# Performance work log

Hardware: AMD Instinct MI355X
Metric: run time of the kernel (lower is better)

Reference implementation:

```python
import jax, jax.numpy as jnp
import numpy as np

DIM = 768
NUM_HEADS = 12
DECAY_RATE = 5.0


def setup_inputs() -> dict:
    key = jax.random.key(0)
    k1, k2, k3, k4 = jax.random.split(key, 4)
    B, N, C = 4, 1024, DIM
    x = jax.random.normal(k1, (B, N, C), dtype=jnp.float32)
    # torch nn.Linear weights: y = x @ W.T ; qkv_bias=False
    qkv_w = jax.random.normal(k2, (3 * C, C), dtype=jnp.float32) * (1.0 / np.sqrt(C))
    proj_w = jax.random.normal(k3, (C, C), dtype=jnp.float32) * (1.0 / np.sqrt(C))
    proj_b = jax.random.normal(k4, (C,), dtype=jnp.float32) * 0.01
    return {"x": x, "qkv_w": qkv_w, "proj_w": proj_w, "proj_b": proj_b, "cur_epoch": 3}


def reference(x, qkv_w, proj_w, proj_b, cur_epoch):
    B, N, C = x.shape
    H = NUM_HEADS
    hd = C // H
    scale = hd ** -0.5

    qkv = (x @ qkv_w.T).reshape(B, N, 3, H, hd).transpose(2, 0, 3, 1, 4)  # [3,B,H,N,hd]
    q, k, v = qkv[0], qkv[1], qkv[2]

    scores = jnp.einsum("bhqd,bhkd->bhqk", q, k) * scale
    logp = jax.nn.log_softmax(scores, axis=-1)
    attn = jnp.exp(logp)  # [B,H,N,N]

    # Per-key entropy: column j of attn flattened over (B,H,N) is renormalized
    # by Categorical; dividing by num_heads cancels under normalization.
    # H(p/s) = log(s) - (1/s) * sum(p * log p)
    s = jnp.sum(attn, axis=(0, 1, 2))                 # [N]
    plogp = jnp.sum(attn * logp, axis=(0, 1, 2))      # [N]
    entropies = jnp.log(s) - plogp / s

    # threshold decay: factor = sum_{i=0}^{cur_epoch-1} decay*exp(-(i+1))
    factor = DECAY_RATE * float(np.sum(np.exp(-(np.arange(cur_epoch) + 1.0))))
    entropy_threshold = float(np.log(C)) - factor

    # attn[:,:,:,keep] @ v[:,:,keep,:] == (attn * mask) @ v  (zeroed columns drop out)
    mask = (entropies <= entropy_threshold).astype(attn.dtype)  # [N]
    out = jnp.einsum("bhqk,bhkd->bhqd", attn * mask[None, None, None, :], v)
    out = out.transpose(0, 2, 1, 3).reshape(B, N, C)
    out = out @ proj_w.T + proj_b
    return out
```

## Files before the change

### kernel.cpp

```cpp
#include <hip/hip_runtime.h>


typedef __bf16 bf16x8 __attribute__((ext_vector_type(8)));
typedef __bf16 bf16x4 __attribute__((ext_vector_type(4)));
typedef float  f32x4  __attribute__((ext_vector_type(4)));

#define MFMA16(a, b, c) __builtin_amdgcn_mfma_f32_16x16x32_bf16((a), (b), (c), 0, 0, 0)
#define LOG2E_8 0.18033688f

__device__ __forceinline__ void ld_glds16(const __bf16* g, __bf16* s) {
  __builtin_amdgcn_global_load_lds(
      (const __attribute__((address_space(1))) unsigned int*)g,
      (__attribute__((address_space(3))) unsigned int*)s, 16, 0, 0);
}

__global__ __launch_bounds__(256) void kc_conv(
    const float* __restrict__ x, const float* __restrict__ qw, const float* __restrict__ pw,
    __bf16* __restrict__ xb, __bf16* __restrict__ qwb, __bf16* __restrict__ pwb,
    float* __restrict__ colSP, int* __restrict__ keepCnt)
{
  const int i = blockIdx.x * 256 + threadIdx.x;
  const float4* src;
  __bf16* dst;
  int j;
  if (i < 786432)       { src = (const float4*)x;  dst = xb;  j = i; }
  else if (i < 1228800) { src = (const float4*)qw; dst = qwb; j = i - 786432; }
  else                  { src = (const float4*)pw; dst = pwb; j = i - 1228800; }
  const float4 f = src[j];
  bf16x4 o;
  o[0] = (__bf16)f.x; o[1] = (__bf16)f.y; o[2] = (__bf16)f.z; o[3] = (__bf16)f.w;
  *(bf16x4*)(dst + 4 * (size_t)j) = o;
  if (i < 2048) colSP[i] = 0.f;
  if (i == 0) *keepCnt = 0;
}

__global__ __launch_bounds__(256) void kg_qkv(
    const __bf16* __restrict__ A, const __bf16* __restrict__ Bm,
    __bf16* __restrict__ qb, __bf16* __restrict__ kb, float* __restrict__ v)
{
  __shared__ __bf16 As[128 * 64];
  __shared__ __bf16 Bs[128 * 64];
  const int tid = threadIdx.x;
  const int w = tid >> 6, lane = tid & 63, quad = lane >> 4, l = lane & 15;
  const int wm = w >> 1, wn = w & 1;
  const int r0 = blockIdx.y * 128, c0 = blockIdx.x * 128;
  const int srow = lane >> 3, skk = (lane & 7) * 8;

  f32x4 acc[4][4] = {};

  for (int k0 = 0; k0 < 768; k0 += 64) {
    if (k0) __syncthreads();
#pragma unroll
    for (int s = 0; s < 4; ++s) {
      const int si = w * 4 + s;
      const int row = si * 8 + srow;
      ld_glds16(A + (size_t)(r0 + row) * 768 + k0 + skk, &As[si * 512]);
      ld_glds16(Bm + (size_t)(c0 + row) * 768 + k0 + skk, &Bs[si * 512]);
    }
    __syncthreads();
#pragma unroll
    for (int kk = 0; kk < 2; ++kk) {
      bf16x8 af[4], bf[4];
#pragma unroll
      for (int t = 0; t < 4; ++t) {
        af[t] = *(const bf16x8*)&As[(wm * 64 + t * 16 + l) * 64 + kk * 32 + quad * 8];
        bf[t] = *(const bf16x8*)&Bs[(wn * 64 + t * 16 + l) * 64 + kk * 32 + quad * 8];
      }
#pragma unroll
      for (int mt = 0; mt < 4; ++mt)
#pragma unroll
        for (int nt = 0; nt < 4; ++nt)
          acc[mt][nt] = MFMA16(af[mt], bf[nt], acc[mt][nt]);
    }
  }

  const int part = c0 / 768;
  const int cbase = c0 % 768;
#pragma unroll
  for (int mt = 0; mt < 4; ++mt) {
#pragma unroll
    for (int nt = 0; nt < 4; ++nt) {
      const int cc = cbase + wn * 64 + nt * 16 + l;
      const int h = cc >> 6, d = cc & 63;
#pragma unroll
      for (int i = 0; i < 4; ++i) {
        const int rg = r0 + wm * 64 + mt * 16 + quad * 4 + i;
        const int b_ = rg >> 10, n = rg & 1023;
        const size_t off = ((size_t)(b_ * 12 + h) * 1024 + n) * 64 + d;
        const float val = acc[mt][nt][i];
        if (part == 0)      qb[off] = (__bf16)val;
        else if (part == 1) kb[off] = (__bf16)val;
        else                v[off]  = val;
      }
    }
  }
}

__global__ __launch_bounds__(512) void ks_fused(
    const __bf16* __restrict__ qb, const __bf16* __restrict__ kb,
    float* __restrict__ lse, float* __restrict__ colSP)
{
  __shared__ float sS[1024];
  __shared__ float sP[1024];
  __shared__ float zrow[64];
  const int tid = threadIdx.x;
  const int w = tid >> 6, lane = tid & 63, quad = lane >> 4, l = lane & 15;
  const int bh = blockIdx.x, r0 = blockIdx.y * 64;
  for (int i = tid; i < 1024; i += 512) { sS[i] = 0.f; sP[i] = 0.f; }
  if (tid < 64) zrow[tid] = 0.f;
  __syncthreads();

  const __bf16* qbase = qb + ((size_t)bh * 1024 + r0 + l) * 64;
  bf16x8 aq0[4], aq1[4];
#pragma unroll
  for (int rt = 0; rt < 4; ++rt) {
    aq0[rt] = *(const bf16x8*)(qbase + rt * 1024 + quad * 8);
    aq1[rt] = *(const bf16x8*)(qbase + rt * 1024 + 32 + quad * 8);
  }
  const __bf16* kfrag = kb + (size_t)bh * 65536 + (size_t)(w * 16 + l) * 64 + quad * 8;
  const f32x4 zero = {0.f, 0.f, 0.f, 0.f};

  bf16x8 kf0 = *(const bf16x8*)(kfrag);
  bf16x8 kf1 = *(const bf16x8*)(kfrag + 32);

  float z[16] = {};
  for (int s = 0; s < 8; ++s) {
    const bf16x8 c0 = kf0, c1 = kf1;
    const int nxt = (s + 1) & 7;
    kf0 = *(const bf16x8*)(kfrag + (size_t)nxt * 8192);
    kf1 = *(const bf16x8*)(kfrag + (size_t)nxt * 8192 + 32);
#pragma unroll
    for (int rt = 0; rt < 4; ++rt) {
      f32x4 acc = MFMA16(aq0[rt], c0, zero);
      acc = MFMA16(aq1[rt], c1, acc);
#pragma unroll
      for (int r = 0; r < 4; ++r) z[rt * 4 + r] += exp2f(acc[r] * LOG2E_8);
    }
  }
#pragma unroll
  for (int off = 1; off < 16; off <<= 1) {
#pragma unroll
    for (int i = 0; i < 16; ++i) z[i] += __shfl_xor(z[i], off);
  }
  if (l == 0) {
#pragma unroll
    for (int rt = 0; rt < 4; ++rt)
#pragma unroll
      for (int r = 0; r < 4; ++r)
        atomicAdd(&zrow[rt * 16 + quad * 4 + r], z[rt * 4 + r]);
  }
  __syncthreads();
  if (tid < 64) lse[bh * 1024 + r0 + tid] = __logf(zrow[tid]);
  float nlb[16], nlg[16];
#pragma unroll
  for (int rt = 0; rt < 4; ++rt) {
#pragma unroll
    for (int r = 0; r < 4; ++r) {
      const float Z = zrow[rt * 16 + quad * 4 + r];
      const float lg = __logf(Z);
      nlg[rt * 4 + r] = -lg;
      nlb[rt * 4 + r] = -lg * 1.44269504f;
    }
  }

  for (int s = 0; s < 8; ++s) {
    const bf16x8 c0 = kf0, c1 = kf1;
    if (s < 7) {
      kf0 = *(const bf16x8*)(kfrag + (size_t)(s + 1) * 8192);
      kf1 = *(const bf16x8*)(kfrag + (size_t)(s + 1) * 8192 + 32);
    }
    float cs = 0.f, cp = 0.f;
#pragma unroll
    for (int rt = 0; rt < 4; ++rt) {
      f32x4 acc = MFMA16(aq0[rt], c0, zero);
      acc = MFMA16(aq1[rt], c1, acc);
#pragma unroll
      for (int r = 0; r < 4; ++r) {
        const float a = acc[r];
        const float t = exp2f(fmaf(a, LOG2E_8, nlb[rt * 4 + r]));
        const float d = fmaf(a, 0.125f, nlg[rt * 4 + r]);
        cs += t;
        cp = fmaf(t, d, cp);
      }
    }
    cs += __shfl_xor(cs, 16); cs += __shfl_xor(cs, 32);
    cp += __shfl_xor(cp, 16); cp += __shfl_xor(cp, 32);
    if (lane < 16) {
      sS[s * 128 + w * 16 + l] += cs;
      sP[s * 128 + w * 16 + l] += cp;
    }
  }
  __syncthreads();
  for (int i = tid; i < 1024; i += 512) {
    atomicAdd(&colSP[i], sS[i]);
    atomicAdd(&colSP[1024 + i], sP[i]);
  }
}

__global__ void k_mask(const float* __restrict__ colSP, const int* __restrict__ cur_epoch,
                       float* __restrict__ mask, int* __restrict__ keepCnt)
{
  const int j = threadIdx.x;
  const float s = colSP[j];
  const float ent = __logf(s) - colSP[1024 + j] / s;
  const int ce = cur_epoch[0];
  float factor = 0.f;
  for (int i = 1; i <= ce; ++i) factor += __expf(-(float)i);
  factor *= 5.0f;
  const float thr = __logf(768.0f) - factor;
  const int keep = (ent <= thr) ? 1 : 0;
  mask[j] = keep ? 1.0f : 0.0f;
  if (keep) atomicAdd(keepCnt, 1);
}

__global__ __launch_bounds__(256) void k_av(
    const __bf16* __restrict__ qb, const __bf16* __restrict__ kb,
    const float* __restrict__ v, const float* __restrict__ lse,
    const float* __restrict__ mask, const int* __restrict__ keepCnt,
    __bf16* __restrict__ ctxb)
{
  if (*keepCnt == 0) return;
  const int tid = threadIdx.x;
  const int bh = blockIdx.x, r0 = blockIdx.y * 32;
  const int b_ = bh / 12, h = bh % 12;
  __shared__ float qs[32][64];
  __shared__ float pbuf[4][8][64];
  for (int i = tid; i < 2048; i += 256)
    qs[i >> 6][i & 63] = (float)qb[((size_t)bh * 1024 + r0) * 64 + i];
  __syncthreads();
  const int w = tid >> 6, l = tid & 63, rb = w * 8;
  float ls[8];
#pragma unroll
  for (int i = 0; i < 8; ++i) ls[i] = lse[bh * 1024 + r0 + rb + i];
  float acc[8] = {};
  for (int chunk = 0; chunk < 16; ++chunk) {
    const float mk = mask[chunk * 64 + l];
    if (__ballot(mk != 0.0f) == 0ull) continue;
    const __bf16* kp = kb + ((size_t)bh * 1024 + chunk * 64 + l) * 64;
    float s[8] = {};
    for (int d0 = 0; d0 < 64; d0 += 8) {
      const bf16x8 kf = *(const bf16x8*)(kp + d0);
#pragma unroll
      for (int dd = 0; dd < 8; ++dd) {
        const float kv = (float)kf[dd];
#pragma unroll
        for (int i = 0; i < 8; ++i) s[i] += qs[rb + i][d0 + dd] * kv;
      }
    }
    __syncthreads();
#pragma unroll
    for (int i = 0; i < 8; ++i)
      pbuf[w][i][l] = __expf(s[i] * 0.125f - ls[i]) * mk;
    __syncthreads();
    const float* vp = v + ((size_t)bh * 1024 + chunk * 64) * 64 + l;
    for (int jj = 0; jj < 64; ++jj) {
      const float vv = vp[(size_t)jj * 64];
#pragma unroll
      for (int i = 0; i < 8; ++i) acc[i] += pbuf[w][i][jj] * vv;
    }
  }
#pragma unroll
  for (int i = 0; i < 8; ++i)
    ctxb[((size_t)(b_ * 1024 + r0 + rb + i)) * 768 + h * 64 + l] = (__bf16)acc[i];
}

__global__ __launch_bounds__(256) void kg_proj(
    const __bf16* __restrict__ A, const __bf16* __restrict__ Bm,
    const float* __restrict__ bias, const int* __restrict__ keepCnt,
    float* __restrict__ out)
{
  const int tid = threadIdx.x;
  const int w = tid >> 6, lane = tid & 63, quad = lane >> 4, l = lane & 15;
  const int r0 = blockIdx.y * 64, c0 = blockIdx.x * 64;
  if (*keepCnt == 0) {
#pragma unroll
    for (int ct = 0; ct < 4; ++ct) {
      const int c = c0 + ct * 16 + l;
      const float bv = bias[c];
#pragma unroll
      for (int i = 0; i < 4; ++i) {
        const int rg = r0 + w * 16 + quad * 4 + i;
        out[(size_t)rg * 768 + c] = bv;
      }
    }
    return;
  }
  __shared__ __bf16 As[64 * 72];
  __shared__ __bf16 Bs[64 * 72];
  const int row = tid >> 3, ko = (tid & 7) * 8;
  const f32x4 zero = {0.f, 0.f, 0.f, 0.f};
  f32x4 acc[4];
#pragma unroll
  for (int ct = 0; ct < 4; ++ct) acc[ct] = zero;

  uint4 a0 = *(const uint4*)(A + (size_t)(r0 + row) * 768 + ko);
  uint4 a1 = *(const uint4*)(A + (size_t)(r0 + row + 32) * 768 + ko);
  uint4 b0 = *(const uint4*)(Bm + (size_t)(c0 + row) * 768 + ko);
  uint4 b1 = *(const uint4*)(Bm + (size_t)(c0 + row + 32) * 768 + ko);

  for (int k0 = 0; k0 < 768; k0 += 64) {
    __syncthreads();
    *(uint4*)&As[row * 72 + ko] = a0;
    *(uint4*)&As[(row + 32) * 72 + ko] = a1;
    *(uint4*)&Bs[row * 72 + ko] = b0;
    *(uint4*)&Bs[(row + 32) * 72 + ko] = b1;
    __syncthreads();
    if (k0 < 704) {
      a0 = *(const uint4*)(A + (size_t)(r0 + row) * 768 + k0 + 64 + ko);
      a1 = *(const uint4*)(A + (size_t)(r0 + row + 32) * 768 + k0 + 64 + ko);
      b0 = *(const uint4*)(Bm + (size_t)(c0 + row) * 768 + k0 + 64 + ko);
      b1 = *(const uint4*)(Bm + (size_t)(c0 + row + 32) * 768 + k0 + 64 + ko);
    }
    const bf16x8 af0 = *(const bf16x8*)&As[(w * 16 + l) * 72 + quad * 8];
    const bf16x8 af1 = *(const bf16x8*)&As[(w * 16 + l) * 72 + 32 + quad * 8];
#pragma unroll
    for (int ct = 0; ct < 4; ++ct) {
      const bf16x8 bf0 = *(const bf16x8*)&Bs[(ct * 16 + l) * 72 + quad * 8];
      const bf16x8 bf1 = *(const bf16x8*)&Bs[(ct * 16 + l) * 72 + 32 + quad * 8];
      acc[ct] = MFMA16(af0, bf0, acc[ct]);
      acc[ct] = MFMA16(af1, bf1, acc[ct]);
    }
  }
#pragma unroll
  for (int ct = 0; ct < 4; ++ct) {
    const int c = c0 + ct * 16 + l;
#pragma unroll
    for (int i = 0; i < 4; ++i) {
      const int rg = r0 + w * 16 + quad * 4 + i;
      out[(size_t)rg * 768 + c] = acc[ct][i] + bias[c];
    }
  }
}

extern "C" void kernel_launch(void* const* d_in, const int* in_sizes, int n_in,
                              void* d_out, int out_size, void* d_ws, size_t ws_size,
                              hipStream_t stream)
{
  const float* x      = (const float*)d_in[0];
  const float* qkv_w  = (const float*)d_in[1];
  const float* proj_w = (const float*)d_in[2];
  const float* proj_b = (const float*)d_in[3];
  const int*   cur_ep = (const int*)d_in[4];

  char* W = (char*)d_ws;
  __bf16* xb    = (__bf16*)(W + 0);
  __bf16* qwb   = (__bf16*)(W + 6291456);
  __bf16* pwb   = (__bf16*)(W + 9830400);
  __bf16* qb    = (__bf16*)(W + 11010048);
  __bf16* kb    = (__bf16*)(W + 17301504);
  float*  v     = (float*) (W + 23592960);
  __bf16* ctxb  = (__bf16*)(W + 36175872);
  float*  lse   = (float*) (W + 42467328);
  float*  mask  = (float*) (W + 42663936);
  int*    keep  = (int*)   (W + 42668032);
  float*  colSP = (float*) (W + 42668544);
  float*  out   = (float*)d_out;

  kc_conv<<<5376, 256, 0, stream>>>(x, qkv_w, proj_w, xb, qwb, pwb, colSP, keep);
  kg_qkv<<<dim3(18, 32), 256, 0, stream>>>(xb, qwb, qb, kb, v);
  ks_fused<<<dim3(48, 16), 512, 0, stream>>>(qb, kb, lse, colSP);
  k_mask<<<1, 1024, 0, stream>>>(colSP, cur_ep, mask, keep);
  k_av<<<dim3(48, 32), 256, 0, stream>>>(qb, kb, v, lse, mask, keep, ctxb);
  kg_proj<<<dim3(12, 64), 256, 0, stream>>>(ctxb, pwb, proj_b, keep, out);
}
```

Before: 159.2 us.

## Split fused score-stats kernel into row-sum, log, and column-stats kernels

The single fused kernel that computed row normalizers and then per-key column sums is split into three kernels. The first accumulates row exp-sums into global memory with atomics, the second takes the log, and the third iterates over query rows with each block owning 16 key columns. This lets column stats be accumulated in registers and drops the shared-memory staging and the block-wide sync. In exchange there are more kernel launches, global atomics, an extra lse pass, and the QK^T product is recomputed as before. Smaller blocks and a larger grid increase parallelism.

```diff
diff --git a/kernel.cpp b/kernel.cpp
--- a/kernel.cpp
+++ b/kernel.cpp
@@ -17,7 +17,7 @@
 __global__ __launch_bounds__(256) void kc_conv(
     const float* __restrict__ x, const float* __restrict__ qw, const float* __restrict__ pw,
     __bf16* __restrict__ xb, __bf16* __restrict__ qwb, __bf16* __restrict__ pwb,
-    float* __restrict__ colSP, int* __restrict__ keepCnt)
+    float* __restrict__ lse, float* __restrict__ colSP, int* __restrict__ keepCnt)
 {
   const int i = blockIdx.x * 256 + threadIdx.x;
   const float4* src;
@@ -30,6 +30,7 @@
   bf16x4 o;
   o[0] = (__bf16)f.x; o[1] = (__bf16)f.y; o[2] = (__bf16)f.z; o[3] = (__bf16)f.w;
   *(bf16x4*)(dst + 4 * (size_t)j) = o;
+  if (i < 49152) lse[i] = 0.f;
   if (i < 2048) colSP[i] = 0.f;
   if (i == 0) *keepCnt = 0;
 }
@@ -96,104 +97,98 @@
   }
 }
 
-__global__ __launch_bounds__(512) void ks_fused(
+__global__ __launch_bounds__(256) void k_zrow(
     const __bf16* __restrict__ qb, const __bf16* __restrict__ kb,
-    float* __restrict__ lse, float* __restrict__ colSP)
-{
-  __shared__ float sS[1024];
-  __shared__ float sP[1024];
-  __shared__ float zrow[64];
+    float* __restrict__ lse)
+{
   const int tid = threadIdx.x;
   const int w = tid >> 6, lane = tid & 63, quad = lane >> 4, l = lane & 15;
-  const int bh = blockIdx.x, r0 = blockIdx.y * 64;
-  for (int i = tid; i < 1024; i += 512) { sS[i] = 0.f; sP[i] = 0.f; }
-  if (tid < 64) zrow[tid] = 0.f;
-  __syncthreads();
-
-  const __bf16* qbase = qb + ((size_t)bh * 1024 + r0 + l) * 64;
-  bf16x8 aq0[4], aq1[4];
-#pragma unroll
-  for (int rt = 0; rt < 4; ++rt) {
-    aq0[rt] = *(const bf16x8*)(qbase + rt * 1024 + quad * 8);
-    aq1[rt] = *(const bf16x8*)(qbase + rt * 1024 + 32 + quad * 8);
-  }
-  const __bf16* kfrag = kb + (size_t)bh * 65536 + (size_t)(w * 16 + l) * 64 + quad * 8;
+  const int bh = blockIdx.x, r0 = blockIdx.y * 16;
+
+  const __bf16* qp = qb + ((size_t)bh * 1024 + r0 + l) * 64;
+  const bf16x8 aq0 = *(const bf16x8*)(qp + quad * 8);
+  const bf16x8 aq1 = *(const bf16x8*)(qp + 32 + quad * 8);
+
+  const __bf16* kp = kb + ((size_t)bh * 1024 + w * 256 + l) * 64 + quad * 8;
   const f32x4 zero = {0.f, 0.f, 0.f, 0.f};
 
-  bf16x8 kf0 = *(const bf16x8*)(kfrag);
-  bf16x8 kf1 = *(const bf16x8*)(kfrag + 32);
-
-  float z[16] = {};
-  for (int s = 0; s < 8; ++s) {
+  bf16x8 kf0 = *(const bf16x8*)(kp);
+  bf16x8 kf1 = *(const bf16x8*)(kp + 32);
+
+  float z[4] = {};
+#pragma unroll 2
+  for (int c = 0; c < 16; ++c) {
     const bf16x8 c0 = kf0, c1 = kf1;
-    const int nxt = (s + 1) & 7;
-    kf0 = *(const bf16x8*)(kfrag + (size_t)nxt * 8192);
-    kf1 = *(const bf16x8*)(kfrag + (size_t)nxt * 8192 + 32);
-#pragma unroll
-    for (int rt = 0; rt < 4; ++rt) {
-      f32x4 acc = MFMA16(aq0[rt], c0, zero);
-      acc = MFMA16(aq1[rt], c1, acc);
-#pragma unroll
-      for (int r = 0; r < 4; ++r) z[rt * 4 + r] += exp2f(acc[r] * LOG2E_8);
-    }
+    const int nxt = (c + 1) & 15;
+    kf0 = *(const bf16x8*)(kp + (size_t)nxt * 1024);
+    kf1 = *(const bf16x8*)(kp + (size_t)nxt * 1024 + 32);
+    f32x4 acc = MFMA16(aq0, c0, zero);
+    acc = MFMA16(aq1, c1, acc);
+#pragma unroll
+    for (int r = 0; r < 4; ++r) z[r] += exp2f(acc[r] * LOG2E_8);
   }
 #pragma unroll
   for (int off = 1; off < 16; off <<= 1) {
 #pragma unroll
-    for (int i = 0; i < 16; ++i) z[i] += __shfl_xor(z[i], off);
+    for (int r = 0; r < 4; ++r) z[r] += __shfl_xor(z[r], off);
   }
   if (l == 0) {
 #pragma unroll
-    for (int rt = 0; rt < 4; ++rt)
-#pragma unroll
-      for (int r = 0; r < 4; ++r)
-        atomicAdd(&zrow[rt * 16 + quad * 4 + r], z[rt * 4 + r]);
-  }
-  __syncthreads();
-  if (tid < 64) lse[bh * 1024 + r0 + tid] = __logf(zrow[tid]);
-  float nlb[16], nlg[16];
-#pragma unroll
-  for (int rt = 0; rt < 4; ++rt) {
+    for (int r = 0; r < 4; ++r)
+      atomicAdd(&lse[bh * 1024 + r0 + quad * 4 + r], z[r]);
+  }
+}
+
+__global__ __launch_bounds__(256) void k_zlog(float* __restrict__ lse)
+{
+  const int i = blockIdx.x * 256 + threadIdx.x;
+  lse[i] = __logf(lse[i]);
+}
+
+__global__ __launch_bounds__(256) void k_colstats(
+    const __bf16* __restrict__ qb, const __bf16* __restrict__ kb,
+    const float* __restrict__ lse, float* __restrict__ colSP)
+{
+  const int tid = threadIdx.x;
+  const int w = tid >> 6, lane = tid & 63, quad = lane >> 4, l = lane & 15;
+  const int bh = blockIdx.x, c0 = blockIdx.y * 16;
+
+  const __bf16* kp = kb + ((size_t)bh * 1024 + c0 + l) * 64;
+  const bf16x8 kf0 = *(const bf16x8*)(kp + quad * 8);
+  const bf16x8 kf1 = *(const bf16x8*)(kp + 32 + quad * 8);
+
+  const __bf16* qp = qb + ((size_t)bh * 1024 + w * 256 + l) * 64 + quad * 8;
+  const float* lsep = lse + bh * 1024 + w * 256 + quad * 4;
+  const f32x4 zero = {0.f, 0.f, 0.f, 0.f};
+
+  bf16x8 aq0 = *(const bf16x8*)(qp);
+  bf16x8 aq1 = *(const bf16x8*)(qp + 32);
+
+  float cs = 0.f, cp = 0.f;
+#pragma unroll 2
+  for (int c = 0; c < 16; ++c) {
+    const bf16x8 a0 = aq0, a1 = aq1;
+    const int nxt = (c + 1) & 15;
+    aq0 = *(const bf16x8*)(qp + (size_t)nxt * 1024);
+    aq1 = *(const bf16x8*)(qp + (size_t)nxt * 1024 + 32);
+    const float4 l4 = *(const float4*)(lsep + c * 16);
+    f32x4 acc = MFMA16(a0, kf0, zero);
+    acc = MFMA16(a1, kf1, acc);
 #pragma unroll
     for (int r = 0; r < 4; ++r) {
-      const float Z = zrow[rt * 16 + quad * 4 + r];
-      const float lg = __logf(Z);
-      nlg[rt * 4 + r] = -lg;
-      nlb[rt * 4 + r] = -lg * 1.44269504f;
-    }
-  }
-
-  for (int s = 0; s < 8; ++s) {
-    const bf16x8 c0 = kf0, c1 = kf1;
-    if (s < 7) {
-      kf0 = *(const bf16x8*)(kfrag + (size_t)(s + 1) * 8192);
-      kf1 = *(const bf16x8*)(kfrag + (size_t)(s + 1) * 8192 + 32);
-    }
-    float cs = 0.f, cp = 0.f;
-#pragma unroll
-    for (int rt = 0; rt < 4; ++rt) {
-      f32x4 acc = MFMA16(aq0[rt], c0, zero);
-      acc = MFMA16(aq1[rt], c1, acc);
-#pragma unroll
-      for (int r = 0; r < 4; ++r) {
-        const float a = acc[r];
-        const float t = exp2f(fmaf(a, LOG2E_8, nlb[rt * 4 + r]));
-        const float d = fmaf(a, 0.125f, nlg[rt * 4 + r]);
-        cs += t;
-        cp = fmaf(t, d, cp);
-      }
-    }
-    cs += __shfl_xor(cs, 16); cs += __shfl_xor(cs, 32);
-    cp += __shfl_xor(cp, 16); cp += __shfl_xor(cp, 32);
-    if (lane < 16) {
-      sS[s * 128 + w * 16 + l] += cs;
-      sP[s * 128 + w * 16 + l] += cp;
-    }
-  }
-  __syncthreads();
-  for (int i = tid; i < 1024; i += 512) {
-    atomicAdd(&colSP[i], sS[i]);
-    atomicAdd(&colSP[1024 + i], sP[i]);
+      const float a = acc[r];
+      const float lr = (r == 0) ? l4.x : (r == 1) ? l4.y : (r == 2) ? l4.z : l4.w;
+      const float d = fmaf(a, 0.125f, -lr);
+      const float t = exp2f(d * 1.44269504f);
+      cs += t;
+      cp = fmaf(t, d, cp);
+    }
+  }
+  cs += __shfl_xor(cs, 16); cs += __shfl_xor(cs, 32);
+  cp += __shfl_xor(cp, 16); cp += __shfl_xor(cp, 32);
+  if (lane < 16) {
+    atomicAdd(&colSP[c0 + l], cs);
+    atomicAdd(&colSP[1024 + c0 + l], cp);
   }
 }
 
@@ -356,9 +351,11 @@
   float*  colSP = (float*) (W + 42668544);
   float*  out   = (float*)d_out;
 
-  kc_conv<<<5376, 256, 0, stream>>>(x, qkv_w, proj_w, xb, qwb, pwb, colSP, keep);
+  kc_conv<<<5376, 256, 0, stream>>>(x, qkv_w, proj_w, xb, qwb, pwb, lse, colSP, keep);
   kg_qkv<<<dim3(18, 32), 256, 0, stream>>>(xb, qwb, qb, kb, v);
-  ks_fused<<<dim3(48, 16), 512, 0, stream>>>(qb, kb, lse, colSP);
+  k_zrow<<<dim3(48, 64), 256, 0, stream>>>(qb, kb, lse);
+  k_zlog<<<192, 256, 0, stream>>>(lse);
+  k_colstats<<<dim3(48, 64), 256, 0, stream>>>(qb, kb, lse, colSP);
   k_mask<<<1, 1024, 0, stream>>>(colSP, cur_ep, mask, keep);
   k_av<<<dim3(48, 32), 256, 0, stream>>>(qb, kb, v, lse, mask, keep, ctxb);
   kg_proj<<<dim3(12, 64), 256, 0, stream>>>(ctxb, pwb, proj_b, keep, out);
```

Result: slower. 222.2 us (+39.5%).
